# Optimization experiments

Hardware: AMD Instinct MI355X
Metric: run time of the kernel (lower is better)

The kernel has to match this reference:

```python
import jax, jax.numpy as jnp
import numpy as np

DIM = 1024
HEADS = 16
HEAD_DIM = DIM // HEADS
RANK = 4
AUDIO_DIM = 768


def _lora(x, A, B):
    # x: [..., in]; A: [rank, in]; B: [out, rank]
    return x + (x @ A.T @ B.T) * (1.0 / RANK)


def setup_inputs() -> dict:
    key = jax.random.key(0)
    ks = jax.random.split(key, 20)
    s = 0.02
    inp = {
        "x": jax.random.normal(ks[0], (1, 4096, DIM), jnp.float32),
        "audio_features": jax.random.normal(ks[1], (1, 1024, AUDIO_DIM), jnp.float32),
        "q_w": jax.random.normal(ks[2], (DIM, DIM), jnp.float32) * s,
        "q_b": jnp.zeros((DIM,), jnp.float32),
        "k_w": jax.random.normal(ks[3], (DIM, DIM), jnp.float32) * s,
        "k_b": jnp.zeros((DIM,), jnp.float32),
        "v_w": jax.random.normal(ks[4], (DIM, DIM), jnp.float32) * s,
        "v_b": jnp.zeros((DIM,), jnp.float32),
        "o_w": jax.random.normal(ks[5], (DIM, DIM), jnp.float32) * s,
        "o_b": jnp.zeros((DIM,), jnp.float32),
        "a_w": jax.random.normal(ks[6], (DIM, AUDIO_DIM), jnp.float32) * s,
        "a_b": jnp.zeros((DIM,), jnp.float32),
        "qA": jax.random.normal(ks[7], (RANK, DIM), jnp.float32) * 0.01,
        "qB": jax.random.normal(ks[8], (DIM, RANK), jnp.float32) * 0.01,
        "kA": jax.random.normal(ks[9], (RANK, DIM), jnp.float32) * 0.01,
        "kB": jax.random.normal(ks[10], (DIM, RANK), jnp.float32) * 0.01,
        "vA": jax.random.normal(ks[11], (RANK, DIM), jnp.float32) * 0.01,
        "vB": jax.random.normal(ks[12], (DIM, RANK), jnp.float32) * 0.01,
    }
    return inp


def reference(x, audio_features, q_w, q_b, k_w, k_b, v_w, v_b, o_w, o_b,
              a_w, a_b, qA, qB, kA, kB, vA, vB):
    B, N, C = x.shape
    # audio projection: Linear(768 -> dim), torch Linear is x @ W.T + b
    audio = audio_features @ a_w.T + a_b  # [B, M, C]
    M = audio.shape[1]

    q = _lora(x @ q_w.T + q_b, qA, qB)      # [B, N, C]
    k = _lora(audio @ k_w.T + k_b, kA, kB)  # [B, M, C]
    v = _lora(audio @ v_w.T + v_b, vA, vB)  # [B, M, C]

    q = q.reshape(B, N, HEADS, HEAD_DIM).transpose(0, 2, 1, 3)  # [B,H,N,d]
    k = k.reshape(B, M, HEADS, HEAD_DIM).transpose(0, 2, 1, 3)  # [B,H,M,d]
    v = v.reshape(B, M, HEADS, HEAD_DIM).transpose(0, 2, 1, 3)  # [B,H,M,d]

    scale = HEAD_DIM ** -0.5
    attn = jnp.einsum('bhnd,bhmd->bhnm', q, k) * scale  # [B,H,N,M]
    attn = jax.nn.softmax(attn, axis=-1)
    out = jnp.einsum('bhnm,bhmd->bhnd', attn, v)        # [B,H,N,d]
    out = out.transpose(0, 2, 1, 3).reshape(B, N, C)
    return out @ o_w.T + o_b
```

## Files before the change

kernel.cpp:

```cpp
#include <hip/hip_runtime.h>
#include <math.h>

#define DIM 1024
#define HEADS 16
#define HD 64
#define QSCALE 0.1803368801111204f

typedef __attribute__((ext_vector_type(8))) short short8;
typedef __attribute__((ext_vector_type(4))) float f32x4;
typedef unsigned short ushort_t;

#define MFMA(a, b, c) __builtin_amdgcn_mfma_f32_16x16x32_bf16(a, b, c, 0, 0, 0)
#define VMCNT(n) asm volatile("s_waitcnt vmcnt(" #n ")" ::: "memory")
#define BARRIER() __builtin_amdgcn_s_barrier()

__device__ __forceinline__ ushort_t f2bf(float f) {
    union { float f; unsigned u; } v; v.f = f;
    unsigned r = v.u + 0x7FFF + ((v.u >> 16) & 1);
    return (ushort_t)(r >> 16);
}
__device__ __forceinline__ void gl2lds16(const void* g, void* l) {
    __builtin_amdgcn_global_load_lds(
        (const __attribute__((address_space(1))) unsigned*)g,
        (__attribute__((address_space(3))) unsigned*)l, 16, 0, 0);
}

#define C_X  1048576
#define C_AF 196608
__global__ __launch_bounds__(256) void prep_cvt(
    const float* __restrict__ x, const float* __restrict__ af,
    const float* __restrict__ aw, const float* __restrict__ ow,
    ushort_t* __restrict__ xb, ushort_t* __restrict__ afb,
    ushort_t* __restrict__ awb, ushort_t* __restrict__ owb,
    const float* __restrict__ qw, const float* __restrict__ kw,
    const float* __restrict__ vw,
    const float* __restrict__ qA, const float* __restrict__ kA,
    const float* __restrict__ vA,
    const float* __restrict__ qB, const float* __restrict__ kB,
    const float* __restrict__ vB,
    const float* __restrict__ qb, const float* __restrict__ kb,
    const float* __restrict__ vb,
    ushort_t* __restrict__ wqe, ushort_t* __restrict__ wke,
    ushort_t* __restrict__ wve, float* __restrict__ beff)
{
    const int b = blockIdx.x, tid = threadIdx.x;
    if (b < 6656) {
        int c = b * 256 + tid;
        const float* s; ushort_t* d; int off;
        if (c < C_X)               { s = x;  d = xb;  off = c; }
        else if (c < C_X + C_AF)   { s = af; d = afb; off = c - C_X; }
        else if (c < C_X + 2*C_AF) { s = aw; d = awb; off = c - C_X - C_AF; }
        else                       { s = ow; d = owb; off = c - C_X - 2*C_AF; }
        float4 v = ((const float4*)s)[off];
        ushort4 o = { f2bf(v.x), f2bf(v.y), f2bf(v.z), f2bf(v.w) };
        ((ushort4*)d)[off] = o;
        return;
    }
    const int pb = b - 6656;
    const int proj = pb >> 6, ib = pb & 63;
    const float* W = proj == 0 ? qw : proj == 1 ? kw : vw;
    const float* A = proj == 0 ? qA : proj == 1 ? kA : vA;
    const float* B = proj == 0 ? qB : proj == 1 ? kB : vB;
    const float* bias = proj == 0 ? qb : proj == 1 ? kb : vb;
    ushort_t* Weff = proj == 0 ? wqe : proj == 1 ? wke : wve;
    const float scale = proj == 0 ? QSCALE : 1.0f;

    const int ic = tid & 15;
    const int oc = tid >> 4;
    const int i = ib * 16 + ic;

    float part[4] = {0.f, 0.f, 0.f, 0.f};
    for (int o = oc * 64; o < oc * 64 + 64; ++o) {
        float wv = W[(size_t)o * 1024 + i];
        part[0] = fmaf(A[o], wv, part[0]);
        part[1] = fmaf(A[1024 + o], wv, part[1]);
        part[2] = fmaf(A[2048 + o], wv, part[2]);
        part[3] = fmaf(A[3072 + o], wv, part[3]);
    }
    __shared__ float red[4][16][16];
    #pragma unroll
    for (int r = 0; r < 4; ++r) red[r][oc][ic] = part[r];
    __syncthreads();
    __shared__ float T1s[4][16];
    if (tid < 64) {
        int r = tid >> 4, icc = tid & 15;
        float s = 0.f;
        #pragma unroll
        for (int u = 0; u < 16; ++u) s += red[r][u][icc];
        T1s[r][icc] = s;
    }
    __syncthreads();
    const float t0 = T1s[0][ic], t1 = T1s[1][ic];
    const float t2 = T1s[2][ic], t3 = T1s[3][ic];
    for (int o = oc * 64; o < oc * 64 + 64; ++o) {
        float4 Bo = *(const float4*)(B + o * 4);
        float wv = W[(size_t)o * 1024 + i];
        float v = wv + 0.25f * (Bo.x*t0 + Bo.y*t1 + Bo.z*t2 + Bo.w*t3);
        Weff[(size_t)o * 1024 + i] = f2bf(v * scale);
    }
    if (ib == 0) {
        float bt[4] = {0.f, 0.f, 0.f, 0.f};
        for (int o = tid; o < 1024; o += 256) {
            float bo = bias[o];
            bt[0] = fmaf(A[o], bo, bt[0]);
            bt[1] = fmaf(A[1024 + o], bo, bt[1]);
            bt[2] = fmaf(A[2048 + o], bo, bt[2]);
            bt[3] = fmaf(A[3072 + o], bo, bt[3]);
        }
        #pragma unroll
        for (int r = 0; r < 4; ++r)
            #pragma unroll
            for (int off = 32; off; off >>= 1) bt[r] += __shfl_xor(bt[r], off);
        __shared__ float btr[4][4];
        if ((tid & 63) == 0) {
            #pragma unroll
            for (int r = 0; r < 4; ++r) btr[r][tid >> 6] = bt[r];
        }
        __syncthreads();
        float b0 = btr[0][0] + btr[0][1] + btr[0][2] + btr[0][3];
        float b1 = btr[1][0] + btr[1][1] + btr[1][2] + btr[1][3];
        float b2 = btr[2][0] + btr[2][1] + btr[2][2] + btr[2][3];
        float b3 = btr[3][0] + btr[3][1] + btr[3][2] + btr[3][3];
        for (int o = tid; o < 1024; o += 256) {
            float4 Bo = *(const float4*)(B + o * 4);
            beff[proj * 1024 + o] =
                (bias[o] + 0.25f * (Bo.x*b0 + Bo.y*b1 + Bo.z*b2 + Bo.w*b3)) * scale;
        }
    }
}

template<int OUTF32>
__device__ __forceinline__ void gemm3p_body(
    char* lds, const ushort_t* __restrict__ A, const ushort_t* __restrict__ W,
    const float* __restrict__ bias, void* __restrict__ C,
    int N, int K, int bm, int bn)
{
    const int tid = threadIdx.x, lane = tid & 63, wv = tid >> 6;
    const int l15 = lane & 15, l4 = lane >> 4;
    const int wm = wv >> 1, wn = wv & 1;

    const ushort_t *Ag[2], *Wg[2];
    #pragma unroll
    for (int c = 0; c < 2; ++c) {
        int f = c * 256 + tid, ra = f >> 2, ga = (f & 3) ^ ((ra >> 1) & 3);
        Ag[c] = A + (size_t)(bm * 128 + ra) * K + ga * 8;
        Wg[c] = W + (size_t)(bn * 128 + ra) * K + ga * 8;
    }
    int aoff[4], woff[4];
    #pragma unroll
    for (int m = 0; m < 4; ++m) {
        int r = wm * 64 + m * 16 + l15;
        aoff[m] = r * 64 + ((l4 ^ ((r >> 1) & 3)) << 4);
    }
    #pragma unroll
    for (int n = 0; n < 4; ++n) {
        int cc = wn * 64 + n * 16 + l15;
        woff[n] = cc * 64 + ((l4 ^ ((cc >> 1) & 3)) << 4);
    }

    auto stage = [&](char* base, int k0) {
        #pragma unroll
        for (int c = 0; c < 2; ++c) {
            gl2lds16(Ag[c] + k0, base + c * 4096 + wv * 1024);
            gl2lds16(Wg[c] + k0, base + 8192 + c * 4096 + wv * 1024);
        }
    };

    short8 fa[4], fw[4];
    auto readfr = [&](const char* base) {
        #pragma unroll
        for (int m = 0; m < 4; ++m) fa[m] = *(const short8*)(base + aoff[m]);
        #pragma unroll
        for (int n = 0; n < 4; ++n) fw[n] = *(const short8*)(base + 8192 + woff[n]);
    };

    f32x4 acc[4][4] = {};
    const int nt = K / 32;

    stage(lds, 0);
    stage(lds + 16384, 32);
    VMCNT(4);
    BARRIER();
    readfr(lds);

    int bcur = 0;
    for (int t = 0; t < nt; ++t) {
        int bnext = bcur + 1; if (bnext == 3) bnext = 0;
        int bpre  = bnext + 1; if (bpre == 3) bpre = 0;
        if (t + 2 < nt) stage(lds + bpre * 16384, (t + 2) * 32);
        #pragma unroll
        for (int m = 0; m < 4; ++m)
            #pragma unroll
            for (int n = 0; n < 4; ++n)
                acc[m][n] = MFMA(fa[m], fw[n], acc[m][n]);
        if (t + 1 < nt) {
            if (t + 2 < nt) { VMCNT(4); } else { VMCNT(0); }
            BARRIER();
            readfr(lds + bnext * 16384);
        }
        bcur = bnext;
    }

    #pragma unroll
    for (int n = 0; n < 4; ++n) {
        int gc = bn * 128 + wn * 64 + n * 16 + l15;
        float bv = bias[gc];
        #pragma unroll
        for (int m = 0; m < 4; ++m) {
            int gr = bm * 128 + wm * 64 + m * 16 + (l4 << 2);
            #pragma unroll
            for (int j = 0; j < 4; ++j) {
                float v = acc[m][n][j] + bv;
                if (OUTF32) ((float*)C)[(size_t)(gr + j) * N + gc] = v;
                else        ((ushort_t*)C)[(size_t)(gr + j) * N + gc] = f2bf(v);
            }
        }
    }
}

template<int OUTF32>
__global__ __launch_bounds__(256) void gemm3p(
    const ushort_t* __restrict__ A, const ushort_t* __restrict__ W,
    const float* __restrict__ bias, void* __restrict__ C, int N, int K)
{
    __shared__ char lds[49152];
    gemm3p_body<OUTF32>(lds, A, W, bias, C, N, K, blockIdx.y, blockIdx.x);
}

__device__ __forceinline__ void audio_body(
    char* lds, const ushort_t* __restrict__ A, const ushort_t* __restrict__ W,
    const float* __restrict__ bias, ushort_t* __restrict__ C, int bm, int bn)
{
    const int K = 768, N = DIM;
    char* As = lds;
    char* Ws = lds + 8192;
    const int tid = threadIdx.x, lane = tid & 63, wv = tid >> 6;
    const int l15 = lane & 15, l4 = lane >> 4;

    int f = tid, ra = f >> 2, ga = (f & 3) ^ ((ra >> 1) & 3);
    const ushort_t* Ag = A + (size_t)(bm * 64 + ra) * K + ga * 8;
    const ushort_t* Wg = W + (size_t)(bn * 64 + ra) * K + ga * 8;

    int aoff, woff[4];
    { int r = wv * 16 + l15; aoff = r * 64 + ((l4 ^ ((r >> 1) & 3)) << 4); }
    #pragma unroll
    for (int n = 0; n < 4; ++n) {
        int cc = n * 16 + l15;
        woff[n] = cc * 64 + ((l4 ^ ((cc >> 1) & 3)) << 4);
    }

    f32x4 acc[4] = {};
    const int nt = K / 32;
    gl2lds16(Ag, As + wv * 1024);
    gl2lds16(Wg, Ws + wv * 1024);

    for (int t = 0; t < nt; ++t) {
        const int buf = t & 1;
        if (t + 1 < nt) {
            const int k1 = (t + 1) * 32;
            gl2lds16(Ag + k1, As + (buf ^ 1) * 4096 + wv * 1024);
            gl2lds16(Wg + k1, Ws + (buf ^ 1) * 4096 + wv * 1024);
            VMCNT(2);
        } else {
            VMCNT(0);
        }
        BARRIER();
        const char* AsB = As + buf * 4096;
        const char* WsB = Ws + buf * 4096;
        short8 fa = *(const short8*)(AsB + aoff);
        short8 fw[4];
        #pragma unroll
        for (int n = 0; n < 4; ++n) fw[n] = *(const short8*)(WsB + woff[n]);
        #pragma unroll
        for (int n = 0; n < 4; ++n) acc[n] = MFMA(fa, fw[n], acc[n]);
        BARRIER();
    }

    const int gr = bm * 64 + wv * 16 + (l4 << 2);
    #pragma unroll
    for (int n = 0; n < 4; ++n) {
        int gc = bn * 64 + n * 16 + l15;
        float bb = bias[gc];
        #pragma unroll
        for (int j = 0; j < 4; ++j)
            C[(size_t)(gr + j) * N + gc] = f2bf(acc[n][j] + bb);
    }
}

__global__ __launch_bounds__(256) void fused_aq(
    const ushort_t* __restrict__ afb, const ushort_t* __restrict__ awb,
    const float* __restrict__ a_b, ushort_t* __restrict__ audio,
    const ushort_t* __restrict__ xb, const ushort_t* __restrict__ wqe,
    const float* __restrict__ beff, ushort_t* __restrict__ qbb)
{
    __shared__ char lds[49152];
    const int b = blockIdx.x;
    if (b < 256) {
        audio_body(lds, afb, awb, a_b, audio, b >> 4, b & 15);
    } else {
        const int i = b - 256;
        gemm3p_body<0>(lds, xb, wqe, beff, qbb, DIM, DIM, i >> 3, i & 7);
    }
}

__global__ __launch_bounds__(256) void gemm2_kv(
    const ushort_t* __restrict__ A, const ushort_t* __restrict__ Wk,
    const ushort_t* __restrict__ Wv, const float* __restrict__ bk,
    const float* __restrict__ bv, ushort_t* __restrict__ Ck,
    ushort_t* __restrict__ CvT)
{
    const int K = DIM;
    __shared__ ushort_t As[2][64 * 32];
    __shared__ ushort_t Ws[2][64 * 32];
    const int tid = threadIdx.x, lane = tid & 63, wv = tid >> 6;
    const int l15 = lane & 15, l4 = lane >> 4;
    const int bm = blockIdx.y;
    const bool isV = blockIdx.x >= 16;
    const int bn = blockIdx.x & 15;
    const ushort_t* W = isV ? Wv : Wk;

    int f = tid, ra = f >> 2, ga = (f & 3) ^ ((ra >> 1) & 3);
    const ushort_t* Ag = A + (size_t)(bm * 64 + ra) * K + ga * 8;
    const ushort_t* Wg = W + (size_t)(bn * 64 + ra) * K + ga * 8;

    int aoff, woff[4];
    { int r = wv * 16 + l15; aoff = r * 64 + ((l4 ^ ((r >> 1) & 3)) << 4); }
    #pragma unroll
    for (int n = 0; n < 4; ++n) {
        int cc = n * 16 + l15;
        woff[n] = cc * 64 + ((l4 ^ ((cc >> 1) & 3)) << 4);
    }

    f32x4 acc[4] = {};
    const int nt = K / 32;
    gl2lds16(Ag, (char*)As + wv * 1024);
    gl2lds16(Wg, (char*)Ws + wv * 1024);

    for (int t = 0; t < nt; ++t) {
        const int buf = t & 1;
        if (t + 1 < nt) {
            const int k1 = (t + 1) * 32;
            gl2lds16(Ag + k1, (char*)As + (buf ^ 1) * 4096 + wv * 1024);
            gl2lds16(Wg + k1, (char*)Ws + (buf ^ 1) * 4096 + wv * 1024);
            VMCNT(2);
        } else {
            VMCNT(0);
        }
        BARRIER();
        const char* AsB = (const char*)As + buf * 4096;
        const char* WsB = (const char*)Ws + buf * 4096;
        short8 fa = *(const short8*)(AsB + aoff);
        short8 fw[4];
        #pragma unroll
        for (int n = 0; n < 4; ++n) fw[n] = *(const short8*)(WsB + woff[n]);
        #pragma unroll
        for (int n = 0; n < 4; ++n) acc[n] = MFMA(fa, fw[n], acc[n]);
        BARRIER();
    }

    const int gr = bm * 64 + wv * 16 + (l4 << 2);
    #pragma unroll
    for (int n = 0; n < 4; ++n) {
        int gc = bn * 64 + n * 16 + l15;
        float bb = (isV ? bv : bk)[gc];
        if (!isV) {
            #pragma unroll
            for (int j = 0; j < 4; ++j)
                Ck[(size_t)(gr + j) * DIM + gc] = f2bf(acc[n][j] + bb);
        } else {
            ushort4 o = { f2bf(acc[n][0] + bb), f2bf(acc[n][1] + bb),
                          f2bf(acc[n][2] + bb), f2bf(acc[n][3] + bb) };
            *(ushort4*)(CvT + (size_t)gc * DIM + gr) = o;
        }
    }
}

__global__ __launch_bounds__(256) void attn3(
    const ushort_t* __restrict__ Qf, const ushort_t* __restrict__ Kf,
    const ushort_t* __restrict__ Vt, ushort_t* __restrict__ AO)
{
    __shared__ char lds[40960];
    char* QsPs = lds;
    char* KsB0 = lds + 8192;
    char* VsB0 = lds + 24576;

    const int tid = threadIdx.x, lane = tid & 63, wv = tid >> 6;
    const int l15 = lane & 15, l4 = lane >> 4;
    const int h = blockIdx.y, qb = blockIdx.x;

    #pragma unroll
    for (int i = 0; i < 2; ++i) {
        int f = i * 256 + tid, q = f >> 3, s = (f & 7) ^ (q & 7);
        gl2lds16(Qf + (size_t)(qb * 64 + q) * DIM + h * HD + s * 8,
                 QsPs + i * 4096 + wv * 1024);
    }
    const int f0 = tid, r0 = f0 >> 3, s0 = (f0 & 7) ^ (r0 & 7);
    const int f1 = 256 + tid, r1 = f1 >> 3, s1 = (f1 & 7) ^ (r1 & 7);
    const ushort_t* Kg0 = Kf + (size_t)r0 * DIM + h * HD + s0 * 8;
    const ushort_t* Kg1 = Kf + (size_t)r1 * DIM + h * HD + s1 * 8;
    const ushort_t* Vg0 = Vt + (size_t)(h * HD + r0) * DIM + s0 * 8;
    const ushort_t* Vg1 = Vt + (size_t)(h * HD + r1) * DIM + s1 * 8;

    int qoff[2], koff[4][2], poff[2];
    #pragma unroll
    for (int ks = 0; ks < 2; ++ks) {
        int r = wv * 16 + l15;
        qoff[ks] = r * 128 + (((ks * 4 + l4) ^ (r & 7)) << 4);
        poff[ks] = wv * 2048 + l15 * 128 + (((ks * 4 + l4) ^ (l15 & 7)) << 4);
    }
    #pragma unroll
    for (int n = 0; n < 4; ++n) {
        int kk = n * 16 + l15;
        #pragma unroll
        for (int ks = 0; ks < 2; ++ks)
            koff[n][ks] = kk * 128 + (((ks * 4 + l4) ^ (kk & 7)) << 4);
    }

    f32x4 acc_o[4] = {};
    float l_loc[4] = {0.f, 0.f, 0.f, 0.f};

    gl2lds16(Kg0, KsB0 + wv * 1024);
    gl2lds16(Kg1, KsB0 + 4096 + wv * 1024);
    gl2lds16(Vg0, VsB0 + wv * 1024);
    gl2lds16(Vg1, VsB0 + 4096 + wv * 1024);
    VMCNT(4);
    BARRIER();
    short8 fq[2];
    #pragma unroll
    for (int ks = 0; ks < 2; ++ks)
        fq[ks] = *(const short8*)(QsPs + qoff[ks]);

    for (int t = 0; t < 16; ++t) {
        const int buf = t & 1;
        if (t < 15) {
            gl2lds16(Kg0 + (size_t)(t + 1) * 64 * DIM,
                     KsB0 + (buf ^ 1) * 8192 + wv * 1024);
            gl2lds16(Kg1 + (size_t)(t + 1) * 64 * DIM,
                     KsB0 + (buf ^ 1) * 8192 + 4096 + wv * 1024);
            gl2lds16(Vg0 + (t + 1) * 64,
                     VsB0 + (buf ^ 1) * 8192 + wv * 1024);
            gl2lds16(Vg1 + (t + 1) * 64,
                     VsB0 + (buf ^ 1) * 8192 + 4096 + wv * 1024);
            VMCNT(4);
        } else {
            VMCNT(0);
        }
        BARRIER();

        const char* KsT = KsB0 + buf * 8192;
        const char* VsT = VsB0 + buf * 8192;

        f32x4 s_acc[4] = {};
        short8 fk[4][2];
        #pragma unroll
        for (int n = 0; n < 4; ++n)
            #pragma unroll
            for (int ks = 0; ks < 2; ++ks)
                fk[n][ks] = *(const short8*)(KsT + koff[n][ks]);
        #pragma unroll
        for (int n = 0; n < 4; ++n)
            #pragma unroll
            for (int ks = 0; ks < 2; ++ks)
                s_acc[n] = MFMA(fq[ks], fk[n][ks], s_acc[n]);

        #pragma unroll
        for (int j = 0; j < 4; ++j) {
            float p0 = exp2f(s_acc[0][j]);
            float p1 = exp2f(s_acc[1][j]);
            float p2 = exp2f(s_acc[2][j]);
            float p3 = exp2f(s_acc[3][j]);
            l_loc[j] += (p0 + p1) + (p2 + p3);
            unsigned pk01, pk23;
            asm("v_cvt_pk_bf16_f32 %0, %1, %2" : "=v"(pk01) : "v"(p0), "v"(p1));
            asm("v_cvt_pk_bf16_f32 %0, %1, %2" : "=v"(pk23) : "v"(p2), "v"(p3));
            int r16 = (l4 << 2) + j;
            int basb = wv * 2048 + r16 * 128;
            int sw = (r16 & 7) << 4;
            int kx = l15 * 2;
            *(ushort_t*)(QsPs + basb + ((kx) ^ sw))      = (ushort_t)pk01;
            *(ushort_t*)(QsPs + basb + ((32 + kx) ^ sw)) = (ushort_t)(pk01 >> 16);
            *(ushort_t*)(QsPs + basb + ((64 + kx) ^ sw)) = (ushort_t)pk23;
            *(ushort_t*)(QsPs + basb + ((96 + kx) ^ sw)) = (ushort_t)(pk23 >> 16);
        }

        short8 pa[2], fv[4][2];
        #pragma unroll
        for (int ks = 0; ks < 2; ++ks)
            pa[ks] = *(const short8*)(QsPs + poff[ks]);
        #pragma unroll
        for (int n = 0; n < 4; ++n)
            #pragma unroll
            for (int ks = 0; ks < 2; ++ks)
                fv[n][ks] = *(const short8*)(VsT + koff[n][ks]);
        #pragma unroll
        for (int dn = 0; dn < 4; ++dn)
            #pragma unroll
            for (int ks = 0; ks < 2; ++ks)
                acc_o[dn] = MFMA(pa[ks], fv[dn][ks], acc_o[dn]);
        BARRIER();
    }

    #pragma unroll
    for (int j = 0; j < 4; ++j) {
        float l = l_loc[j];
        l += __shfl_xor(l, 1);
        l += __shfl_xor(l, 2);
        l += __shfl_xor(l, 4);
        l += __shfl_xor(l, 8);
        float inv = 1.0f / l;
        int q = qb * 64 + wv * 16 + (l4 << 2) + j;
        #pragma unroll
        for (int dn = 0; dn < 4; ++dn)
            AO[(size_t)q * DIM + h * HD + dn * 16 + l15] =
                f2bf(acc_o[dn][j] * inv);
    }
}

extern "C" void kernel_launch(void* const* d_in, const int* in_sizes, int n_in,
                              void* d_out, int out_size, void* d_ws, size_t ws_size,
                              hipStream_t stream)
{
    const float* x   = (const float*)d_in[0];
    const float* af  = (const float*)d_in[1];
    const float* q_w = (const float*)d_in[2];
    const float* q_b = (const float*)d_in[3];
    const float* k_w = (const float*)d_in[4];
    const float* k_b = (const float*)d_in[5];
    const float* v_w = (const float*)d_in[6];
    const float* v_b = (const float*)d_in[7];
    const float* o_w = (const float*)d_in[8];
    const float* o_b = (const float*)d_in[9];
    const float* a_w = (const float*)d_in[10];
    const float* a_b = (const float*)d_in[11];
    const float* qA  = (const float*)d_in[12];
    const float* qB  = (const float*)d_in[13];
    const float* kA  = (const float*)d_in[14];
    const float* kB  = (const float*)d_in[15];
    const float* vA  = (const float*)d_in[16];
    const float* vB  = (const float*)d_in[17];
    float* out = (float*)d_out;

    const int N = 4096;

    char* w = (char*)d_ws;
    auto alloc = [&](size_t bytes) {
        char* p = w; w += (bytes + 255) & ~(size_t)255; return p;
    };
    ushort_t* xb   = (ushort_t*)alloc((size_t)N * DIM * 2);
    ushort_t* afb  = (ushort_t*)alloc((size_t)1024 * 768 * 2);
    ushort_t* awb  = (ushort_t*)alloc((size_t)DIM * 768 * 2);
    ushort_t* owb  = (ushort_t*)alloc((size_t)DIM * DIM * 2);
    ushort_t* wqe  = (ushort_t*)alloc((size_t)DIM * DIM * 2);
    ushort_t* wke  = (ushort_t*)alloc((size_t)DIM * DIM * 2);
    ushort_t* wve  = (ushort_t*)alloc((size_t)DIM * DIM * 2);
    ushort_t* audio= (ushort_t*)alloc((size_t)1024 * DIM * 2);
    ushort_t* qbb  = (ushort_t*)alloc((size_t)N * DIM * 2);
    ushort_t* kbb  = (ushort_t*)alloc((size_t)1024 * DIM * 2);
    ushort_t* vt   = (ushort_t*)alloc((size_t)1024 * DIM * 2);
    ushort_t* ao   = (ushort_t*)alloc((size_t)N * DIM * 2);
    float* beff = (float*)alloc((size_t)3 * 1024 * 4);

    prep_cvt<<<6848, 256, 0, stream>>>(
        x, af, a_w, o_w, xb, afb, awb, owb,
        q_w, k_w, v_w, qA, kA, vA, qB, kB, vB, q_b, k_b, v_b,
        wqe, wke, wve, beff);
    fused_aq<<<512, 256, 0, stream>>>(afb, awb, a_b, audio, xb, wqe, beff, qbb);
    gemm2_kv<<<dim3(32, 16), 256, 0, stream>>>(audio, wke, wve,
                                               beff + 1024, beff + 2048, kbb, vt);
    attn3<<<dim3(N / 64, HEADS), 256, 0, stream>>>(qbb, kbb, vt, ao);
    gemm3p<1><<<dim3(8, 32), 256, 0, stream>>>(ao, owb, o_b, out, DIM, DIM);
}
```

Before: 227.3 us.

## Split LoRA weight folding into two kernels with coalesced row-wise reads

The LoRA-into-weight folding is moved out of the conversion kernel and split in two. The first kernel computes per-chunk partial A·W products with coalesced float4 row reads and writes them to a scratch buffer. A second 48-block kernel reduces the partials and writes the effective bf16 weights with vectorized stores. This replaces the old strided 16-column reads of W, which coalesced poorly, at the cost of an extra launch, a scratch round trip, and a tail of only 48 blocks in the second kernel.

```diff
diff --git a/kernel.cpp b/kernel.cpp
--- a/kernel.cpp
+++ b/kernel.cpp
@@ -27,7 +27,7 @@
 
 #define C_X  1048576
 #define C_AF 196608
-__global__ __launch_bounds__(256) void prep_cvt(
+__global__ __launch_bounds__(256) void prep1(
     const float* __restrict__ x, const float* __restrict__ af,
     const float* __restrict__ aw, const float* __restrict__ ow,
     ushort_t* __restrict__ xb, ushort_t* __restrict__ afb,
@@ -36,12 +36,7 @@
     const float* __restrict__ vw,
     const float* __restrict__ qA, const float* __restrict__ kA,
     const float* __restrict__ vA,
-    const float* __restrict__ qB, const float* __restrict__ kB,
-    const float* __restrict__ vB,
-    const float* __restrict__ qb, const float* __restrict__ kb,
-    const float* __restrict__ vb,
-    ushort_t* __restrict__ wqe, ushort_t* __restrict__ wke,
-    ushort_t* __restrict__ wve, float* __restrict__ beff)
+    float* __restrict__ part)
 {
     const int b = blockIdx.x, tid = threadIdx.x;
     if (b < 6656) {
@@ -57,48 +52,82 @@
         return;
     }
     const int pb = b - 6656;
-    const int proj = pb >> 6, ib = pb & 63;
+    const int proj = pb >> 4, chunk = pb & 15;
+    const float* W = proj == 0 ? qw : proj == 1 ? kw : vw;
+    const float* A = proj == 0 ? qA : proj == 1 ? kA : vA;
+    const float4* W4 = (const float4*)W;
+
+    float4 acc0 = {0,0,0,0}, acc1 = {0,0,0,0}, acc2 = {0,0,0,0}, acc3 = {0,0,0,0};
+    const int o0 = chunk * 64;
+    for (int o = o0; o < o0 + 64; ++o) {
+        float4 wrow = W4[o * 256 + tid];
+        float a0 = A[o], a1 = A[1024 + o], a2 = A[2048 + o], a3 = A[3072 + o];
+        acc0.x += a0 * wrow.x; acc0.y += a0 * wrow.y; acc0.z += a0 * wrow.z; acc0.w += a0 * wrow.w;
+        acc1.x += a1 * wrow.x; acc1.y += a1 * wrow.y; acc1.z += a1 * wrow.z; acc1.w += a1 * wrow.w;
+        acc2.x += a2 * wrow.x; acc2.y += a2 * wrow.y; acc2.z += a2 * wrow.z; acc2.w += a2 * wrow.w;
+        acc3.x += a3 * wrow.x; acc3.y += a3 * wrow.y; acc3.z += a3 * wrow.z; acc3.w += a3 * wrow.w;
+    }
+    float4* P4 = (float4*)part;
+    P4[(pb * 4 + 0) * 256 + tid] = acc0;
+    P4[(pb * 4 + 1) * 256 + tid] = acc1;
+    P4[(pb * 4 + 2) * 256 + tid] = acc2;
+    P4[(pb * 4 + 3) * 256 + tid] = acc3;
+}
+
+__global__ __launch_bounds__(256) void prep2(
+    const float* __restrict__ qw, const float* __restrict__ kw,
+    const float* __restrict__ vw,
+    const float* __restrict__ qA, const float* __restrict__ kA,
+    const float* __restrict__ vA,
+    const float* __restrict__ qB, const float* __restrict__ kB,
+    const float* __restrict__ vB,
+    const float* __restrict__ qb, const float* __restrict__ kb,
+    const float* __restrict__ vb,
+    const float* __restrict__ part,
+    ushort_t* __restrict__ wqe, ushort_t* __restrict__ wke,
+    ushort_t* __restrict__ wve, float* __restrict__ beff)
+{
+    const int b = blockIdx.x, tid = threadIdx.x;
+    const int proj = b >> 4, chunk = b & 15;
     const float* W = proj == 0 ? qw : proj == 1 ? kw : vw;
     const float* A = proj == 0 ? qA : proj == 1 ? kA : vA;
     const float* B = proj == 0 ? qB : proj == 1 ? kB : vB;
     const float* bias = proj == 0 ? qb : proj == 1 ? kb : vb;
     ushort_t* Weff = proj == 0 ? wqe : proj == 1 ? wke : wve;
     const float scale = proj == 0 ? QSCALE : 1.0f;
-
-    const int ic = tid & 15;
-    const int oc = tid >> 4;
-    const int i = ib * 16 + ic;
-
-    float part[4] = {0.f, 0.f, 0.f, 0.f};
-    for (int o = oc * 64; o < oc * 64 + 64; ++o) {
-        float wv = W[(size_t)o * 1024 + i];
-        part[0] = fmaf(A[o], wv, part[0]);
-        part[1] = fmaf(A[1024 + o], wv, part[1]);
-        part[2] = fmaf(A[2048 + o], wv, part[2]);
-        part[3] = fmaf(A[3072 + o], wv, part[3]);
-    }
-    __shared__ float red[4][16][16];
-    #pragma unroll
-    for (int r = 0; r < 4; ++r) red[r][oc][ic] = part[r];
+    const float4* W4 = (const float4*)W;
+    const float4* P4 = (const float4*)part;
+
+    __shared__ float T1s[4096];
+    #pragma unroll
+    for (int r = 0; r < 4; ++r) {
+        float4 s = {0, 0, 0, 0};
+        for (int blk = 0; blk < 16; ++blk) {
+            float4 p = P4[((proj * 16 + blk) * 4 + r) * 256 + tid];
+            s.x += p.x; s.y += p.y; s.z += p.z; s.w += p.w;
+        }
+        *(float4*)(T1s + r * 1024 + tid * 4) = s;
+    }
     __syncthreads();
-    __shared__ float T1s[4][16];
-    if (tid < 64) {
-        int r = tid >> 4, icc = tid & 15;
-        float s = 0.f;
-        #pragma unroll
-        for (int u = 0; u < 16; ++u) s += red[r][u][icc];
-        T1s[r][icc] = s;
-    }
-    __syncthreads();
-    const float t0 = T1s[0][ic], t1 = T1s[1][ic];
-    const float t2 = T1s[2][ic], t3 = T1s[3][ic];
-    for (int o = oc * 64; o < oc * 64 + 64; ++o) {
+
+    float4 t0 = *(const float4*)(T1s + tid * 4);
+    float4 t1 = *(const float4*)(T1s + 1024 + tid * 4);
+    float4 t2 = *(const float4*)(T1s + 2048 + tid * 4);
+    float4 t3 = *(const float4*)(T1s + 3072 + tid * 4);
+
+    const int o0 = chunk * 64;
+    for (int o = o0; o < o0 + 64; ++o) {
+        float4 wrow = W4[o * 256 + tid];
         float4 Bo = *(const float4*)(B + o * 4);
-        float wv = W[(size_t)o * 1024 + i];
-        float v = wv + 0.25f * (Bo.x*t0 + Bo.y*t1 + Bo.z*t2 + Bo.w*t3);
-        Weff[(size_t)o * 1024 + i] = f2bf(v * scale);
-    }
-    if (ib == 0) {
+        ushort4 out;
+        out.x = f2bf((wrow.x + 0.25f * (Bo.x*t0.x + Bo.y*t1.x + Bo.z*t2.x + Bo.w*t3.x)) * scale);
+        out.y = f2bf((wrow.y + 0.25f * (Bo.x*t0.y + Bo.y*t1.y + Bo.z*t2.y + Bo.w*t3.y)) * scale);
+        out.z = f2bf((wrow.z + 0.25f * (Bo.x*t0.z + Bo.y*t1.z + Bo.z*t2.z + Bo.w*t3.z)) * scale);
+        out.w = f2bf((wrow.w + 0.25f * (Bo.x*t0.w + Bo.y*t1.w + Bo.z*t2.w + Bo.w*t3.w)) * scale);
+        *(ushort4*)(Weff + (size_t)o * 1024 + tid * 4) = out;
+    }
+
+    if (chunk == 0) {
         float bt[4] = {0.f, 0.f, 0.f, 0.f};
         for (int o = tid; o < 1024; o += 256) {
             float bo = bias[o];
@@ -558,12 +587,15 @@
     ushort_t* kbb  = (ushort_t*)alloc((size_t)1024 * DIM * 2);
     ushort_t* vt   = (ushort_t*)alloc((size_t)1024 * DIM * 2);
     ushort_t* ao   = (ushort_t*)alloc((size_t)N * DIM * 2);
+    float* part = (float*)alloc((size_t)48 * 4 * 1024 * 4);
     float* beff = (float*)alloc((size_t)3 * 1024 * 4);
 
-    prep_cvt<<<6848, 256, 0, stream>>>(
+    prep1<<<6704, 256, 0, stream>>>(
         x, af, a_w, o_w, xb, afb, awb, owb,
+        q_w, k_w, v_w, qA, kA, vA, part);
+    prep2<<<48, 256, 0, stream>>>(
         q_w, k_w, v_w, qA, kA, vA, qB, kB, vB, q_b, k_b, v_b,
-        wqe, wke, wve, beff);
+        part, wqe, wke, wve, beff);
     fused_aq<<<512, 256, 0, stream>>>(afb, awb, a_b, audio, xb, wqe, beff, qbb);
     gemm2_kv<<<dim3(32, 16), 256, 0, stream>>>(audio, wke, wve,
                                                beff + 1024, beff + 2048, kbb, vt);
```

After: 230.6 us. Within noise of the previous version (+1.5%).
